# Kernel tuning notes

Hardware: AMD Instinct MI355X
Metric: run time of the kernel (lower is better)

## Reference

```python
import jax, jax.numpy as jnp
import numpy as np

N_NODES = 50000
N_EDGES = 800000
IN_DIM = 128
HID = 128
BN_EPS = 1e-5


def setup_inputs() -> dict:
    key = jax.random.key(0)
    ks = jax.random.split(key, 8)
    x = jax.random.normal(ks[0], (N_NODES, IN_DIM), dtype=jnp.float32)
    edge_index = jax.random.randint(ks[1], (2, N_EDGES), 0, N_NODES, dtype=jnp.int64)
    s1 = 1.0 / np.sqrt(IN_DIM)
    s2 = 1.0 / np.sqrt(HID)
    return {
        'x': x,
        'edge_index': edge_index,
        'w1_0': jax.random.normal(ks[2], (IN_DIM, HID), dtype=jnp.float32) * s1,
        'b1_0': jnp.zeros((HID,), dtype=jnp.float32),
        'w2_0': jax.random.normal(ks[3], (HID, HID), dtype=jnp.float32) * s2,
        'b2_0': jnp.zeros((HID,), dtype=jnp.float32),
        'g_0': jnp.ones((HID,), dtype=jnp.float32),
        'be_0': jnp.zeros((HID,), dtype=jnp.float32),
        'w1_1': jax.random.normal(ks[4], (HID, HID), dtype=jnp.float32) * s2,
        'b1_1': jnp.zeros((HID,), dtype=jnp.float32),
        'w2_1': jax.random.normal(ks[5], (HID, HID), dtype=jnp.float32) * s2,
        'b2_1': jnp.zeros((HID,), dtype=jnp.float32),
        'g_1': jnp.ones((HID,), dtype=jnp.float32),
        'be_1': jnp.zeros((HID,), dtype=jnp.float32),
    }


def _gin_layer(h, src, dst, w1, b1, w2, b2, g, be):
    # GINConv with eps=0: MLP(h_i + sum_{j->i} h_j); scatter-add over targets
    agg = jax.ops.segment_sum(h[src], dst, num_segments=N_NODES)
    z = h + agg
    z = jax.nn.relu(z @ w1 + b1) @ w2 + b2
    # BatchNorm1d (training mode: batch stats over nodes, biased variance)
    mu = jnp.mean(z, axis=0)
    var = jnp.mean(jnp.square(z - mu), axis=0)
    z = (z - mu) * jax.lax.rsqrt(var + BN_EPS) * g + be
    return jax.nn.relu(z)


def reference(x, edge_index, w1_0, b1_0, w2_0, b2_0, g_0, be_0,
              w1_1, b1_1, w2_1, b2_1, g_1, be_1):
    src, dst = edge_index[0], edge_index[1]
    h = _gin_layer(x, src, dst, w1_0, b1_0, w2_0, b2_0, g_0, be_0)
    # dropout p=0.0 -> no-op between layers
    h = _gin_layer(h, src, dst, w1_1, b1_1, w2_1, b2_1, g_1, be_1)
    return h
```

## Files before the change

kernel.cpp:

```cpp
#include <hip/hip_runtime.h>
#include <hip/hip_bf16.h>

#define HID 128
#define LDA 136
#define CAP 64

typedef __attribute__((ext_vector_type(8))) short frag8;
typedef __attribute__((ext_vector_type(4))) float f32x4;

__device__ inline float bf2f(unsigned short u) {
    return __uint_as_float(((unsigned int)u) << 16);
}
__device__ inline unsigned short f2bf(float f) {
    __hip_bfloat16 h = __float2bfloat16(f);
    return __builtin_bit_cast(unsigned short, h);
}
__device__ inline float4 u4tof4(ushort4 u) {
    return make_float4(bf2f(u.x), bf2f(u.y), bf2f(u.z), bf2f(u.w));
}
__device__ inline ushort4 f4tou4(float4 f) {
    ushort4 u; u.x = f2bf(f.x); u.y = f2bf(f.y); u.z = f2bf(f.z); u.w = f2bf(f.w);
    return u;
}
__device__ inline float4 bnrelu4(float4 u, float4 s, float4 b) {
    float4 r;
    r.x = fmaxf(fmaf(u.x, s.x, b.x), 0.0f);
    r.y = fmaxf(fmaf(u.y, s.y, b.y), 0.0f);
    r.z = fmaxf(fmaf(u.z, s.z, b.z), 0.0f);
    r.w = fmaxf(fmaf(u.w, s.w, b.w), 0.0f);
    return r;
}
__device__ inline void acc4(float4& a, float4 u) {
    a.x += u.x; a.y += u.y; a.z += u.z; a.w += u.w;
}

__global__ __launch_bounds__(256) void mega_prep_k(
    const float* __restrict__ x, unsigned short* __restrict__ B0,
    const float* __restrict__ w0, const float* __restrict__ w1,
    const float* __restrict__ w2, const float* __restrict__ w3,
    unsigned short* __restrict__ wt,
    const int* __restrict__ src, const int* __restrict__ dst,
    int* __restrict__ cursor, int* __restrict__ eidx,
    int n_edges, long total4, int fb, int vb)
{
    const int bid = blockIdx.x;
    const int t = threadIdx.x;
    if (bid < fb) {
        int e = bid * 256 + t;
        if (e < n_edges) {
            int d = dst[e];
            int p = atomicAdd(&cursor[d], 1);
            if (p < CAP) eidx[d * CAP + p] = src[e];
        }
    } else if (bid < fb + vb) {
        long i = (long)(bid - fb) * 256 + t;
        if (i < total4)
            ((ushort4*)B0)[i] = f4tou4(((const float4*)x)[i]);
    } else {
        int w_id = bid - fb - vb;
        const float* w = (w_id == 0) ? w0 : (w_id == 1) ? w1 : (w_id == 2) ? w2 : w3;
        unsigned short* o = wt + (size_t)w_id * 128 * 128;
        for (int i = 0; i < 64; i++) {
            int idx = t + i * 256;
            int k = idx >> 7, nn = idx & 127;
            o[nn * 128 + k] = f2bf(w[idx]);
        }
    }
}

template<bool BN>
__global__ __launch_bounds__(256) void gather_t(
    const unsigned short* __restrict__ h, unsigned short* __restrict__ z,
    const int* __restrict__ cnt, const int* __restrict__ eidx,
    const float* __restrict__ S, const float* __restrict__ g,
    const float* __restrict__ be, float inv_n, int n)
{
    __shared__ float lsc[BN ? 128 : 1], lsh[BN ? 128 : 1];
    if (BN) {
        int t = threadIdx.x;
        if (t < 128) {
            float mu = S[t] * inv_n;
            float var = fmaf(-mu, mu, S[128 + t] * inv_n);
            float s = g[t] * rsqrtf(var + 1e-5f);
            lsc[t] = s;
            lsh[t] = fmaf(-mu, s, be[t]);
        }
        __syncthreads();
    }

    int tid = blockIdx.x * 256 + threadIdx.x;
    int v = tid >> 5;
    if (v >= n) return;
    int q = (tid & 31) << 2;

    float4 scv, shv;
    if (BN) {
        scv = *(const float4*)(lsc + q);
        shv = *(const float4*)(lsh + q);
    }

    float4 a0 = u4tof4(*(const ushort4*)(h + (size_t)v * HID + q));
    if (BN) a0 = bnrelu4(a0, scv, shv);
    float4 a1 = make_float4(0.f, 0.f, 0.f, 0.f);

    const int* bucket = eidx + (size_t)v * CAP;
    int deg = cnt[v];
    if (deg > CAP) deg = CAP;

    int i = 0;
    for (; i + 8 <= deg; i += 8) {
        int s0 = bucket[i + 0], s1 = bucket[i + 1];
        int s2 = bucket[i + 2], s3 = bucket[i + 3];
        int s4 = bucket[i + 4], s5 = bucket[i + 5];
        int s6 = bucket[i + 6], s7 = bucket[i + 7];
        float4 u0 = u4tof4(*(const ushort4*)(h + (size_t)s0 * HID + q));
        float4 u1 = u4tof4(*(const ushort4*)(h + (size_t)s1 * HID + q));
        float4 u2 = u4tof4(*(const ushort4*)(h + (size_t)s2 * HID + q));
        float4 u3 = u4tof4(*(const ushort4*)(h + (size_t)s3 * HID + q));
        float4 u4 = u4tof4(*(const ushort4*)(h + (size_t)s4 * HID + q));
        float4 u5 = u4tof4(*(const ushort4*)(h + (size_t)s5 * HID + q));
        float4 u6 = u4tof4(*(const ushort4*)(h + (size_t)s6 * HID + q));
        float4 u7 = u4tof4(*(const ushort4*)(h + (size_t)s7 * HID + q));
        if (BN) {
            u0 = bnrelu4(u0, scv, shv); u1 = bnrelu4(u1, scv, shv);
            u2 = bnrelu4(u2, scv, shv); u3 = bnrelu4(u3, scv, shv);
            u4 = bnrelu4(u4, scv, shv); u5 = bnrelu4(u5, scv, shv);
            u6 = bnrelu4(u6, scv, shv); u7 = bnrelu4(u7, scv, shv);
        }
        acc4(a0, u0); acc4(a1, u1); acc4(a0, u2); acc4(a1, u3);
        acc4(a0, u4); acc4(a1, u5); acc4(a0, u6); acc4(a1, u7);
    }
    for (; i + 4 <= deg; i += 4) {
        int s0 = bucket[i + 0], s1 = bucket[i + 1];
        int s2 = bucket[i + 2], s3 = bucket[i + 3];
        float4 u0 = u4tof4(*(const ushort4*)(h + (size_t)s0 * HID + q));
        float4 u1 = u4tof4(*(const ushort4*)(h + (size_t)s1 * HID + q));
        float4 u2 = u4tof4(*(const ushort4*)(h + (size_t)s2 * HID + q));
        float4 u3 = u4tof4(*(const ushort4*)(h + (size_t)s3 * HID + q));
        if (BN) {
            u0 = bnrelu4(u0, scv, shv); u1 = bnrelu4(u1, scv, shv);
            u2 = bnrelu4(u2, scv, shv); u3 = bnrelu4(u3, scv, shv);
        }
        acc4(a0, u0); acc4(a1, u1); acc4(a0, u2); acc4(a1, u3);
    }
    for (; i < deg; i++) {
        float4 u = u4tof4(*(const ushort4*)(h + (size_t)bucket[i] * HID + q));
        if (BN) u = bnrelu4(u, scv, shv);
        acc4(a0, u);
    }
    acc4(a0, a1);
    *(ushort4*)(z + (size_t)v * HID + q) = f4tou4(a0);
}

__global__ __launch_bounds__(256) void mlp_k(
    unsigned short* __restrict__ Z,
    const unsigned short* __restrict__ W1t, const float* __restrict__ b1,
    const unsigned short* __restrict__ W2t, const float* __restrict__ b2,
    float* __restrict__ S, int n_rows)
{
    __shared__ unsigned short Hs[128 * LDA];
    __shared__ float red[1024];

    const int t = threadIdx.x;
    const int row0 = blockIdx.x * 128;
    const int wave = t >> 6;
    const int lane = t & 63;
    const int l15  = lane & 15;
    const int quad = lane >> 4;

    const int r0 = row0 + wave * 32 + l15;
    const int r1 = r0 + 16;
    const int rs0 = (r0 < n_rows) ? r0 : 0;
    const int rs1 = (r1 < n_rows) ? r1 : 0;
    frag8 a0[4], a1[4];
    #pragma unroll
    for (int kk = 0; kk < 4; kk++) {
        a0[kk] = *(const frag8*)(Z + (size_t)rs0 * HID + kk * 32 + quad * 8);
        a1[kk] = *(const frag8*)(Z + (size_t)rs1 * HID + kk * 32 + quad * 8);
    }

    f32x4 acc[2][8];
    #pragma unroll
    for (int tr = 0; tr < 2; tr++)
        #pragma unroll
        for (int tc = 0; tc < 8; tc++)
            acc[tr][tc] = (f32x4){0.f, 0.f, 0.f, 0.f};

    #pragma unroll
    for (int kk = 0; kk < 4; kk++) {
        int ko = kk * 32 + quad * 8;
        #pragma unroll
        for (int tc = 0; tc < 8; tc++) {
            frag8 b = *(const frag8*)(W1t + (size_t)(tc * 16 + l15) * HID + ko);
            acc[0][tc] = __builtin_amdgcn_mfma_f32_16x16x32_bf16(a0[kk], b, acc[0][tc], 0, 0, 0);
            acc[1][tc] = __builtin_amdgcn_mfma_f32_16x16x32_bf16(a1[kk], b, acc[1][tc], 0, 0, 0);
        }
    }

    const int wrow = wave * 32;
    #pragma unroll
    for (int tc = 0; tc < 8; tc++) {
        const int col = tc * 16 + l15;
        const float bc = b1[col];
        #pragma unroll
        for (int tr = 0; tr < 2; tr++) {
            #pragma unroll
            for (int r = 0; r < 4; r++) {
                int lrow = wrow + tr * 16 + quad * 4 + r;
                Hs[lrow * LDA + col] = f2bf(fmaxf(acc[tr][tc][r] + bc, 0.f));
            }
        }
    }
    __syncthreads();

    #pragma unroll
    for (int kk = 0; kk < 4; kk++) {
        a0[kk] = *(const frag8*)(Hs + (wave * 32 + l15) * LDA + kk * 32 + quad * 8);
        a1[kk] = *(const frag8*)(Hs + (wave * 32 + 16 + l15) * LDA + kk * 32 + quad * 8);
    }
    #pragma unroll
    for (int tr = 0; tr < 2; tr++)
        #pragma unroll
        for (int tc = 0; tc < 8; tc++)
            acc[tr][tc] = (f32x4){0.f, 0.f, 0.f, 0.f};

    #pragma unroll
    for (int kk = 0; kk < 4; kk++) {
        int ko = kk * 32 + quad * 8;
        #pragma unroll
        for (int tc = 0; tc < 8; tc++) {
            frag8 b = *(const frag8*)(W2t + (size_t)(tc * 16 + l15) * HID + ko);
            acc[0][tc] = __builtin_amdgcn_mfma_f32_16x16x32_bf16(a0[kk], b, acc[0][tc], 0, 0, 0);
            acc[1][tc] = __builtin_amdgcn_mfma_f32_16x16x32_bf16(a1[kk], b, acc[1][tc], 0, 0, 0);
        }
    }

    #pragma unroll
    for (int tc = 0; tc < 8; tc++) {
        const int col = tc * 16 + l15;
        const float bc = b2[col];
        float s = 0.f, sq = 0.f;
        #pragma unroll
        for (int tr = 0; tr < 2; tr++) {
            #pragma unroll
            for (int r = 0; r < 4; r++) {
                int grow = row0 + wrow + tr * 16 + quad * 4 + r;
                float o = acc[tr][tc][r] + bc;
                if (grow < n_rows) {
                    s += o; sq = fmaf(o, o, sq);
                    Z[(size_t)grow * HID + col] = f2bf(o);
                }
            }
        }
        s  += __shfl_xor(s, 16);  s  += __shfl_xor(s, 32);
        sq += __shfl_xor(sq, 16); sq += __shfl_xor(sq, 32);
        if (lane < 16) {
            red[wave * 128 + col] = s;
            red[512 + wave * 128 + col] = sq;
        }
    }
    __syncthreads();
    {
        int which = t >> 7, c = t & 127;
        const float* rp = red + which * 512;
        atomicAdd(&S[which * 128 + c],
                  rp[c] + rp[128 + c] + rp[256 + c] + rp[384 + c]);
    }
}

__global__ __launch_bounds__(256) void bn_apply_f32_k(
    const unsigned short* __restrict__ z, const float* __restrict__ S,
    const float* __restrict__ g, const float* __restrict__ be,
    float* __restrict__ out, float inv_n, long total4)
{
    __shared__ float lsc[128], lsh[128];
    int t = threadIdx.x;
    if (t < 128) {
        float mu = S[t] * inv_n;
        float var = fmaf(-mu, mu, S[128 + t] * inv_n);
        float s = g[t] * rsqrtf(var + 1e-5f);
        lsc[t] = s;
        lsh[t] = fmaf(-mu, s, be[t]);
    }
    __syncthreads();

    long i = blockIdx.x * 256L + t;
    if (i >= total4) return;
    float4 v = u4tof4(((const ushort4*)z)[i]);
    int c0 = ((int)(i & 31)) * 4;
    v.x = fmaxf(fmaf(v.x, lsc[c0 + 0], lsh[c0 + 0]), 0.0f);
    v.y = fmaxf(fmaf(v.y, lsc[c0 + 1], lsh[c0 + 1]), 0.0f);
    v.z = fmaxf(fmaf(v.z, lsc[c0 + 2], lsh[c0 + 2]), 0.0f);
    v.w = fmaxf(fmaf(v.w, lsc[c0 + 3], lsh[c0 + 3]), 0.0f);
    ((float4*)out)[i] = v;
}

extern "C" void kernel_launch(void* const* d_in, const int* in_sizes, int n_in,
                              void* d_out, int out_size, void* d_ws, size_t ws_size,
                              hipStream_t stream)
{
    const float* x    = (const float*)d_in[0];
    const int*   ei   = (const int*)d_in[1];
    const float* w1_0 = (const float*)d_in[2];
    const float* b1_0 = (const float*)d_in[3];
    const float* w2_0 = (const float*)d_in[4];
    const float* b2_0 = (const float*)d_in[5];
    const float* g_0  = (const float*)d_in[6];
    const float* be_0 = (const float*)d_in[7];
    const float* w1_1 = (const float*)d_in[8];
    const float* b1_1 = (const float*)d_in[9];
    const float* w2_1 = (const float*)d_in[10];
    const float* b2_1 = (const float*)d_in[11];
    const float* g_1  = (const float*)d_in[12];
    const float* be_1 = (const float*)d_in[13];
    float* OUT = (float*)d_out;

    const int n       = in_sizes[0] / HID;
    const int n_edges = in_sizes[1] / 2;
    const int* src = ei;
    const int* dst = ei + n_edges;
    const float inv_n = 1.0f / (float)n;

    char* p = (char*)d_ws;
    unsigned short* B0 = (unsigned short*)p;  p += (size_t)n * HID * sizeof(short);
    unsigned short* B1 = (unsigned short*)p;  p += (size_t)n * HID * sizeof(short);
    unsigned short* Wt = (unsigned short*)p;  p += (size_t)4 * 128 * 128 * sizeof(short);
    int*   cursor = (int*)p;    p += (size_t)n * sizeof(int);
    float* S0     = (float*)p;  p += 256 * sizeof(float);
    float* S1     = (float*)p;  p += 256 * sizeof(float);
    int*   eidx   = (int*)p;    p += (size_t)n * CAP * sizeof(int);

    dim3 blk(256);
    const long total4 = (long)n * (HID / 4);
    const int vb = (int)((total4 + 255) / 256);
    const int fb = (n_edges + 255) / 256;
    const int gb = (n * 32 + 255) / 256;
    const int mlp_blocks = (n + 127) / 128;

    hipMemsetAsync(cursor, 0, (size_t)n * sizeof(int) + 512 * sizeof(float), stream);
    mega_prep_k<<<fb + vb + 4, blk, 0, stream>>>(
        x, B0, w1_0, w2_0, w1_1, w2_1, Wt, src, dst, cursor, eidx,
        n_edges, total4, fb, vb);

    gather_t<false><<<gb, blk, 0, stream>>>(B0, B1, cursor, eidx,
                                            nullptr, nullptr, nullptr, inv_n, n);
    mlp_k<<<mlp_blocks, blk, 0, stream>>>(B1, Wt, b1_0, Wt + 16384, b2_0, S0, n);

    gather_t<true><<<gb, blk, 0, stream>>>(B1, B0, cursor, eidx,
                                           S0, g_0, be_0, inv_n, n);
    mlp_k<<<mlp_blocks, blk, 0, stream>>>(B0, Wt + 2 * 16384, b1_1,
                                          Wt + 3 * 16384, b2_1, S1, n);
    bn_apply_f32_k<<<vb, blk, 0, stream>>>(B0, S1, g_1, be_1, OUT, inv_n, total4);
}
```

Before: 293.9 us.

## Bin edges by 16-node destination groups and build per-node lists in LDS

```diff
diff --git a/kernel.cpp b/kernel.cpp
--- a/kernel.cpp
+++ b/kernel.cpp
@@ -3,6 +3,9 @@
 
 #define HID 128
 #define LDA 136
+#define BINSH 4
+#define BINSZ 16
+#define ECAP 512
 #define CAP 64
 
 typedef __attribute__((ext_vector_type(8))) short frag8;
@@ -15,12 +18,12 @@
     __hip_bfloat16 h = __float2bfloat16(f);
     return __builtin_bit_cast(unsigned short, h);
 }
-__device__ inline float4 u4tof4(ushort4 u) {
-    return make_float4(bf2f(u.x), bf2f(u.y), bf2f(u.z), bf2f(u.w));
-}
 __device__ inline ushort4 f4tou4(float4 f) {
     ushort4 u; u.x = f2bf(f.x); u.y = f2bf(f.y); u.z = f2bf(f.z); u.w = f2bf(f.w);
     return u;
+}
+__device__ inline float4 u4tof4(ushort4 u) {
+    return make_float4(bf2f(u.x), bf2f(u.y), bf2f(u.z), bf2f(u.w));
 }
 __device__ inline float4 bnrelu4(float4 u, float4 s, float4 b) {
     float4 r;
@@ -40,7 +43,7 @@
     const float* __restrict__ w2, const float* __restrict__ w3,
     unsigned short* __restrict__ wt,
     const int* __restrict__ src, const int* __restrict__ dst,
-    int* __restrict__ cursor, int* __restrict__ eidx,
+    int* __restrict__ binCursorP, int* __restrict__ binned,
     int n_edges, long total4, int fb, int vb)
 {
     const int bid = blockIdx.x;
@@ -49,8 +52,10 @@
         int e = bid * 256 + t;
         if (e < n_edges) {
             int d = dst[e];
-            int p = atomicAdd(&cursor[d], 1);
-            if (p < CAP) eidx[d * CAP + p] = src[e];
+            int bin = d >> BINSH;
+            int p = atomicAdd(&binCursorP[bin * 16], 1);
+            if (p < ECAP)
+                binned[(size_t)bin * ECAP + p] = (src[e] << BINSH) | (d & (BINSZ - 1));
         }
     } else if (bid < fb + vb) {
         long i = (long)(bid - fb) * 256 + t;
@@ -69,29 +74,45 @@
 }
 
 template<bool BN>
-__global__ __launch_bounds__(256) void gather_t(
+__global__ __launch_bounds__(512) void gather_bin_k(
     const unsigned short* __restrict__ h, unsigned short* __restrict__ z,
-    const int* __restrict__ cnt, const int* __restrict__ eidx,
+    const int* __restrict__ binCursorP, const int* __restrict__ binned,
     const float* __restrict__ S, const float* __restrict__ g,
     const float* __restrict__ be, float inv_n, int n)
 {
+    __shared__ int Ls[ECAP];
+    __shared__ int cnt16[BINSZ];
+    __shared__ int perNode[BINSZ * CAP];
     __shared__ float lsc[BN ? 128 : 1], lsh[BN ? 128 : 1];
-    if (BN) {
-        int t = threadIdx.x;
-        if (t < 128) {
-            float mu = S[t] * inv_n;
-            float var = fmaf(-mu, mu, S[128 + t] * inv_n);
-            float s = g[t] * rsqrtf(var + 1e-5f);
-            lsc[t] = s;
-            lsh[t] = fmaf(-mu, s, be[t]);
-        }
-        __syncthreads();
-    }
-
-    int tid = blockIdx.x * 256 + threadIdx.x;
-    int v = tid >> 5;
+
+    const int t = threadIdx.x;
+    const int bin = blockIdx.x;
+    const int v0 = bin << BINSH;
+
+    if (t < BINSZ) cnt16[t] = 0;
+    if (BN && t < 128) {
+        float mu = S[t] * inv_n;
+        float var = fmaf(-mu, mu, S[128 + t] * inv_n);
+        float s = g[t] * rsqrtf(var + 1e-5f);
+        lsc[t] = s;
+        lsh[t] = fmaf(-mu, s, be[t]);
+    }
+    int cnt = min(binCursorP[bin * 16], ECAP);
+    for (int j = t; j < cnt; j += 512) Ls[j] = binned[(size_t)bin * ECAP + j];
+    __syncthreads();
+
+    for (int j = t; j < cnt; j += 512) {
+        int pa = Ls[j];
+        int node = pa & (BINSZ - 1);
+        int p = atomicAdd(&cnt16[node], 1);
+        if (p < CAP) perNode[node * CAP + p] = pa >> BINSH;
+    }
+    __syncthreads();
+
+    const int vl = t >> 5;
+    const int v = v0 + vl;
     if (v >= n) return;
-    int q = (tid & 31) << 2;
+    const int q = (t & 31) << 2;
 
     float4 scv, shv;
     if (BN) {
@@ -103,9 +124,8 @@
     if (BN) a0 = bnrelu4(a0, scv, shv);
     float4 a1 = make_float4(0.f, 0.f, 0.f, 0.f);
 
-    const int* bucket = eidx + (size_t)v * CAP;
-    int deg = cnt[v];
-    if (deg > CAP) deg = CAP;
+    const int* bucket = perNode + vl * CAP;
+    int deg = min(cnt16[vl], CAP);
 
     int i = 0;
     for (; i + 8 <= deg; i += 8) {
@@ -320,34 +340,35 @@
     const int* src = ei;
     const int* dst = ei + n_edges;
     const float inv_n = 1.0f / (float)n;
+    const int n_bins = (n + BINSZ - 1) / BINSZ;
 
     char* p = (char*)d_ws;
     unsigned short* B0 = (unsigned short*)p;  p += (size_t)n * HID * sizeof(short);
     unsigned short* B1 = (unsigned short*)p;  p += (size_t)n * HID * sizeof(short);
     unsigned short* Wt = (unsigned short*)p;  p += (size_t)4 * 128 * 128 * sizeof(short);
-    int*   cursor = (int*)p;    p += (size_t)n * sizeof(int);
-    float* S0     = (float*)p;  p += 256 * sizeof(float);
-    float* S1     = (float*)p;  p += 256 * sizeof(float);
-    int*   eidx   = (int*)p;    p += (size_t)n * CAP * sizeof(int);
+    int*   binCursorP = (int*)p;  p += (size_t)n_bins * 16 * sizeof(int);
+    float* S0         = (float*)p;  p += 256 * sizeof(float);
+    float* S1         = (float*)p;  p += 256 * sizeof(float);
+    int*   binned     = (int*)p;    p += (size_t)n_bins * ECAP * sizeof(int);
 
     dim3 blk(256);
     const long total4 = (long)n * (HID / 4);
     const int vb = (int)((total4 + 255) / 256);
     const int fb = (n_edges + 255) / 256;
-    const int gb = (n * 32 + 255) / 256;
     const int mlp_blocks = (n + 127) / 128;
 
-    hipMemsetAsync(cursor, 0, (size_t)n * sizeof(int) + 512 * sizeof(float), stream);
+    hipMemsetAsync(binCursorP, 0,
+                   (size_t)n_bins * 16 * sizeof(int) + 512 * sizeof(float), stream);
     mega_prep_k<<<fb + vb + 4, blk, 0, stream>>>(
-        x, B0, w1_0, w2_0, w1_1, w2_1, Wt, src, dst, cursor, eidx,
+        x, B0, w1_0, w2_0, w1_1, w2_1, Wt, src, dst, binCursorP, binned,
         n_edges, total4, fb, vb);
 
-    gather_t<false><<<gb, blk, 0, stream>>>(B0, B1, cursor, eidx,
-                                            nullptr, nullptr, nullptr, inv_n, n);
+    gather_bin_k<false><<<n_bins, dim3(512), 0, stream>>>(
+        B0, B1, binCursorP, binned, nullptr, nullptr, nullptr, inv_n, n);
     mlp_k<<<mlp_blocks, blk, 0, stream>>>(B1, Wt, b1_0, Wt + 16384, b2_0, S0, n);
 
-    gather_t<true><<<gb, blk, 0, stream>>>(B1, B0, cursor, eidx,
-                                           S0, g_0, be_0, inv_n, n);
+    gather_bin_k<true><<<n_bins, dim3(512), 0, stream>>>(
+        B1, B0, binCursorP, binned, S0, g_0, be_0, inv_n, n);
     mlp_k<<<mlp_blocks, blk, 0, stream>>>(B0, Wt + 2 * 16384, b1_1,
                                           Wt + 3 * 16384, b2_1, S1, n);
     bn_apply_f32_k<<<vb, blk, 0, stream>>>(B0, S1, g_1, be_1, OUT, inv_n, total4);
```

Measured after the change: 283.9 us. -3.4%, faster.
